# Optimization experiments

Measured on AMD Instinct MI355X. Metric: run time of the kernel, lower is better.

## Reference

```python
import jax, jax.numpy as jnp
import numpy as np

BATCH, LEN, N_STATE, D_MODEL = 16, 512, 64, 256
DT_MIN, DT_MAX = 1e-3, 1e-1


def setup_inputs() -> dict:
    key = jax.random.key(0)
    ks = jax.random.split(key, 8)
    log_dt = jax.random.uniform(ks[7], (1,), jnp.float32) * (np.log(DT_MAX) - np.log(DT_MIN)) + np.log(DT_MIN)
    return {
        "u": jax.random.normal(ks[0], (BATCH, LEN, D_MODEL), jnp.float32),
        "Lambda_re": jax.random.normal(ks[1], (N_STATE,), jnp.float32),
        "Lambda_im": jax.random.normal(ks[2], (N_STATE,), jnp.float32),
        "B_re": jax.random.normal(ks[3], (N_STATE,), jnp.float32),
        "B_im": jax.random.normal(ks[4], (N_STATE,), jnp.float32),
        "P_re": jax.random.normal(ks[5], (N_STATE, D_MODEL), jnp.float32),
        "P_im": jax.random.normal(ks[6], (N_STATE, D_MODEL), jnp.float32),
        "log_dt": log_dt,
    }


def reference(u, Lambda_re, Lambda_im, B_re, B_im, P_re, P_im, log_dt):
    # Diagonal (S4D-style) SSM recurrence, per-channel independent states.
    dt = jnp.exp(log_dt[0])
    Lam = Lambda_re + 1j * Lambda_im                      # (N,)
    a = jnp.exp(dt * (-jnp.exp(Lam)))                     # (N,) discrete diagonal transition
    Bd = (dt * (B_re + 1j * B_im)).astype(jnp.complex64)  # (N,)
    C = (P_re + 1j * P_im).astype(jnp.complex64)          # (N, D)
    a = a.astype(jnp.complex64)

    def step(x, u_t):
        # x: (B, N, D) complex state, u_t: (B, D) real input at this timestep
        x = a[None, :, None] * x + Bd[None, :, None] * u_t[:, None, :].astype(jnp.complex64)
        y = jnp.einsum('nd,bnd->bd', C, x)                # contract state dim
        return x, y

    x0 = jnp.zeros((u.shape[0], a.shape[0], u.shape[2]), dtype=jnp.complex64)
    _, ys = jax.lax.scan(step, x0, jnp.swapaxes(u, 0, 1))  # ys: (L, B, D)
    return jnp.swapaxes(ys, 0, 1).real                     # (B, L, D) float32
```

## Files before the change

### kernel.cpp

```cpp
#include <hip/hip_runtime.h>

#define BATCH  16
#define LEN    512
#define NSTATE 64
#define DMODEL 256
#define TB     32
#define WAVES  4

__global__ __launch_bounds__(WAVES * 64, 4)
void s4d_scan_kernel(const float* __restrict__ u,
                     const float* __restrict__ Lre_p, const float* __restrict__ Lim_p,
                     const float* __restrict__ Bre_p, const float* __restrict__ Bim_p,
                     const float* __restrict__ Pre_p, const float* __restrict__ Pim_p,
                     const float* __restrict__ logdt_p,
                     float* __restrict__ y)
{
    __shared__ float cb[WAVES][NSTATE][TB + 1];

    const int tid  = threadIdx.x;
    const int lane = tid & 63;
    const int widx = tid >> 6;
    const int wid  = blockIdx.x * WAVES + widx;
    const int b    = wid >> 8;
    const int d    = wid & 255;

    const float dt  = expf(logdt_p[0]);
    const float Lre = Lre_p[lane];
    const float Lim = Lim_p[lane];
    const float eL  = expf(Lre);
    const float wre = -eL * cosf(Lim);
    const float wim = -eL * sinf(Lim);
    const float mag = expf(dt * wre);
    const float are = mag * cosf(dt * wim);
    const float aim = mag * sinf(dt * wim);
    const float Bdre = dt * Bre_p[lane];
    const float Bdim = dt * Bim_p[lane];
    const float Pre  = Pre_p[lane * DMODEL + d];
    const float Pim  = Pim_p[lane * DMODEL + d];
    const float Gre = Pre * Bdre - Pim * Bdim;
    const float Gim = Pre * Bdim + Pim * Bdre;

    float zre = 0.f, zim = 0.f;

    const float* up = u + (size_t)b * LEN * DMODEL + d;
    float*       yp = y + (size_t)b * LEN * DMODEL + d;

    const int tl = lane & 31;
    const int h  = lane >> 5;

    for (int t0 = 0; t0 < LEN; t0 += TB) {
        const float ureg = up[(t0 + tl) * DMODEL];

        #pragma unroll
        for (int tau = 0; tau < TB; ++tau) {
            const float us = __uint_as_float(
                __builtin_amdgcn_readlane(__float_as_uint(ureg), tau));
            const float nzre = fmaf(are, zre, fmaf(-aim, zim, Gre * us));
            const float nzim = fmaf(are, zim, fmaf( aim, zre, Gim * us));
            zre = nzre;
            zim = nzim;
            cb[widx][lane][tau] = zre;
        }
        __syncthreads();

        float s = 0.f;
        #pragma unroll
        for (int j = 0; j < 32; ++j)
            s += cb[widx][32 * h + j][tl];
        s += __shfl_xor(s, 32, 64);
        if (lane < 32)
            yp[(t0 + tl) * DMODEL] = s;
        __syncthreads();
    }
}

extern "C" void kernel_launch(void* const* d_in, const int* in_sizes, int n_in,
                              void* d_out, int out_size, void* d_ws, size_t ws_size,
                              hipStream_t stream) {
    const float* u      = (const float*)d_in[0];
    const float* Lre    = (const float*)d_in[1];
    const float* Lim    = (const float*)d_in[2];
    const float* Bre    = (const float*)d_in[3];
    const float* Bim    = (const float*)d_in[4];
    const float* Pre    = (const float*)d_in[5];
    const float* Pim    = (const float*)d_in[6];
    const float* logdt  = (const float*)d_in[7];
    float* y = (float*)d_out;

    const int nblocks = (BATCH * DMODEL) / WAVES;
    s4d_scan_kernel<<<nblocks, WAVES * 64, 0, stream>>>(
        u, Lre, Lim, Bre, Bim, Pre, Pim, logdt, y);
}
```

Baseline: 38.14 us.

## Prefetch next 64-step input chunk, halve waves per block, pad LDS rows by two

Each lane now loads a 64-timestep input chunk and prefetches the next chunk into a register while the current one is scanned, so global load latency overlaps the recurrence. WAVES drops from 4 to 2, which doubles the block count and narrows each __syncthreads barrier. LDS row padding changes from 1 to 2 so pairs of adjacent stores can be merged. The risks are a stride-34 layout that may add bank conflicts on the column reads, and higher register pressure.

Measured after the change: 43.25 us. +13.4%, slower.

```diff
diff --git a/kernel.cpp b/kernel.cpp
--- a/kernel.cpp
+++ b/kernel.cpp
@@ -5,7 +5,8 @@
 #define NSTATE 64
 #define DMODEL 256
 #define TB     32
-#define WAVES  4
+#define WAVES  2
+#define PAD    2
 
 __global__ __launch_bounds__(WAVES * 64, 4)
 void s4d_scan_kernel(const float* __restrict__ u,
@@ -15,7 +16,7 @@
                      const float* __restrict__ logdt_p,
                      float* __restrict__ y)
 {
-    __shared__ float cb[WAVES][NSTATE][TB + 1];
+    __shared__ float cb[WAVES][NSTATE][TB + PAD];
 
     const int tid  = threadIdx.x;
     const int lane = tid & 63;
@@ -48,29 +49,41 @@
     const int tl = lane & 31;
     const int h  = lane >> 5;
 
-    for (int t0 = 0; t0 < LEN; t0 += TB) {
-        const float ureg = up[(t0 + tl) * DMODEL];
+    float ucur = up[lane * DMODEL];
+
+    for (int m = 0; m < LEN / 64; ++m) {
+        float unext = 0.f;
+        if (m + 1 < LEN / 64)
+            unext = up[((m + 1) * 64 + lane) * DMODEL];
 
         #pragma unroll
-        for (int tau = 0; tau < TB; ++tau) {
-            const float us = __uint_as_float(
-                __builtin_amdgcn_readlane(__float_as_uint(ureg), tau));
-            const float nzre = fmaf(are, zre, fmaf(-aim, zim, Gre * us));
-            const float nzim = fmaf(are, zim, fmaf( aim, zre, Gim * us));
-            zre = nzre;
-            zim = nzim;
-            cb[widx][lane][tau] = zre;
+        for (int half = 0; half < 2; ++half) {
+            #pragma unroll
+            for (int tau = 0; tau < TB; tau += 2) {
+                const float us0 = __uint_as_float(
+                    __builtin_amdgcn_readlane(__float_as_uint(ucur), half * 32 + tau));
+                const float r0 = fmaf(are, zre, fmaf(-aim, zim, Gre * us0));
+                const float i0 = fmaf(are, zim, fmaf( aim, zre, Gim * us0));
+                const float us1 = __uint_as_float(
+                    __builtin_amdgcn_readlane(__float_as_uint(ucur), half * 32 + tau + 1));
+                const float r1 = fmaf(are, r0, fmaf(-aim, i0, Gre * us1));
+                const float i1 = fmaf(are, i0, fmaf( aim, r0, Gim * us1));
+                zre = r1; zim = i1;
+                cb[widx][lane][tau]     = r0;
+                cb[widx][lane][tau + 1] = r1;
+            }
+            __syncthreads();
+
+            float s = 0.f;
+            #pragma unroll
+            for (int j = 0; j < 32; ++j)
+                s += cb[widx][32 * h + j][tl];
+            s += __shfl_xor(s, 32, 64);
+            if (lane < 32)
+                yp[(m * 64 + half * 32 + tl) * DMODEL] = s;
+            __syncthreads();
         }
-        __syncthreads();
-
-        float s = 0.f;
-        #pragma unroll
-        for (int j = 0; j < 32; ++j)
-            s += cb[widx][32 * h + j][tl];
-        s += __shfl_xor(s, 32, 64);
-        if (lane < 32)
-            yp[(t0 + tl) * DMODEL] = s;
-        __syncthreads();
+        ucur = unext;
     }
 }
 
```

## Replace sequential SSM scan with precomputed convolution kernel and direct FIR

Applied to the files above, without the earlier changes.

The diagonal SSM recurrence becomes an explicit causal convolution. A first kernel builds K[tau,d] = Re(sum_n C[n,d] * Bd[n] * a[n]^tau) into workspace, and a second kernel computes each output tile of 16 timesteps as a register-blocked FIR over all past inputs. This removes the serial dependency chain along the sequence and the LDS reduction over states. In exchange the FIR does O(L^2) work per channel and load is uneven across tiles, since late tiles loop far longer than early ones. Computing a^tau through exp and sincos rather than repeated multiplication may also shift numerics slightly.

New measurement: 51.26 us. 34.4% more time.

```diff
diff --git a/kernel.cpp b/kernel.cpp
--- a/kernel.cpp
+++ b/kernel.cpp
@@ -1,93 +1,123 @@
 #include <hip/hip_runtime.h>
 
-#define BATCH  16
-#define LEN    512
-#define NSTATE 64
-#define DMODEL 256
-#define TB     32
-#define WAVES  4
+#define B_    16
+#define L_    512
+#define N_    64
+#define D_    256
+#define T_    16
+#define NT    (L_ / T_)
+#define KROWS (L_ + T_)
+#define GUARD 4
 
-__global__ __launch_bounds__(WAVES * 64, 4)
-void s4d_scan_kernel(const float* __restrict__ u,
-                     const float* __restrict__ Lre_p, const float* __restrict__ Lim_p,
-                     const float* __restrict__ Bre_p, const float* __restrict__ Bim_p,
-                     const float* __restrict__ Pre_p, const float* __restrict__ Pim_p,
-                     const float* __restrict__ logdt_p,
-                     float* __restrict__ y)
+__global__ __launch_bounds__(256)
+void build_K(const float* __restrict__ Lre_p, const float* __restrict__ Lim_p,
+             const float* __restrict__ Bre_p, const float* __restrict__ Bim_p,
+             const float* __restrict__ Pre_p, const float* __restrict__ Pim_p,
+             const float* __restrict__ logdt_p,
+             float* __restrict__ Kpad)
 {
-    __shared__ float cb[WAVES][NSTATE][TB + 1];
+    __shared__ float U[N_], V[N_];
+    const int row = blockIdx.x;
+    const int tau = row - T_;
+    const int d   = threadIdx.x;
 
-    const int tid  = threadIdx.x;
-    const int lane = tid & 63;
-    const int widx = tid >> 6;
-    const int wid  = blockIdx.x * WAVES + widx;
-    const int b    = wid >> 8;
-    const int d    = wid & 255;
+    if (tau < 0) {
+        Kpad[row * D_ + d] = 0.f;
+        return;
+    }
 
-    const float dt  = expf(logdt_p[0]);
-    const float Lre = Lre_p[lane];
-    const float Lim = Lim_p[lane];
-    const float eL  = expf(Lre);
-    const float wre = -eL * cosf(Lim);
-    const float wim = -eL * sinf(Lim);
-    const float mag = expf(dt * wre);
-    const float are = mag * cosf(dt * wim);
-    const float aim = mag * sinf(dt * wim);
-    const float Bdre = dt * Bre_p[lane];
-    const float Bdim = dt * Bim_p[lane];
-    const float Pre  = Pre_p[lane * DMODEL + d];
-    const float Pim  = Pim_p[lane * DMODEL + d];
-    const float Gre = Pre * Bdre - Pim * Bdim;
-    const float Gim = Pre * Bdim + Pim * Bdre;
+    const float dt = expf(logdt_p[0]);
+    if (d < N_) {
+        const float Lre = Lre_p[d], Lim = Lim_p[d];
+        const float eL  = expf(Lre);
+        const float wre = -eL * cosf(Lim);
+        const float wim = -eL * sinf(Lim);
+        const float ft  = (float)tau;
+        const float er  = expf(ft * dt * wre);
+        float sn, cs;
+        sincosf(ft * dt * wim, &sn, &cs);
+        const float Ar = er * cs, Ai = er * sn;
+        const float Bdre = dt * Bre_p[d], Bdim = dt * Bim_p[d];
+        U[d] = Bdre * Ar - Bdim * Ai;
+        V[d] = Bdim * Ar + Bdre * Ai;
+    }
+    __syncthreads();
 
-    float zre = 0.f, zim = 0.f;
+    float acc = 0.f;
+    #pragma unroll 8
+    for (int n = 0; n < N_; ++n)
+        acc = fmaf(Pre_p[n * D_ + d], U[n],
+              fmaf(-Pim_p[n * D_ + d], V[n], acc));
+    Kpad[row * D_ + d] = acc;
+}
 
-    const float* up = u + (size_t)b * LEN * DMODEL + d;
-    float*       yp = y + (size_t)b * LEN * DMODEL + d;
+__global__ __launch_bounds__(256)
+void conv_fir(const float* __restrict__ u, const float* __restrict__ Kpad,
+              float* __restrict__ y)
+{
+    const int bid = blockIdx.x;
+    const int k   = (NT - 1) - (bid >> 4);
+    const int b   = bid & (B_ - 1);
+    const int d   = threadIdx.x;
 
-    const int tl = lane & 31;
-    const int h  = lane >> 5;
+    const float* ub = u + ((size_t)b * L_) * D_ + d;
+    const float* Kb = Kpad + d;
+    float*       yb = y + ((size_t)b * L_ + k * T_) * D_ + d;
 
-    for (int t0 = 0; t0 < LEN; t0 += TB) {
-        const float ureg = up[(t0 + tl) * DMODEL];
+    const int send = T_ * (k + 1);
+    const int r0   = T_ * k + T_;
 
+    float W[16];
+    #pragma unroll
+    for (int j = 1; j < 16; ++j) W[j] = Kb[(r0 + j) * D_];
+    float kr[4], ur[4];
+    #pragma unroll
+    for (int p = 0; p < 4; ++p) {
+        kr[p] = Kb[(r0 - p) * D_];
+        ur[p] = ub[p * D_];
+    }
+    float acc[16];
+    #pragma unroll
+    for (int j = 0; j < 16; ++j) acc[j] = 0.f;
+
+    for (int s0 = 0; s0 < send; s0 += 16) {
         #pragma unroll
-        for (int tau = 0; tau < TB; ++tau) {
-            const float us = __uint_as_float(
-                __builtin_amdgcn_readlane(__float_as_uint(ureg), tau));
-            const float nzre = fmaf(are, zre, fmaf(-aim, zim, Gre * us));
-            const float nzim = fmaf(are, zim, fmaf( aim, zre, Gim * us));
-            zre = nzre;
-            zim = nzim;
-            cb[widx][lane][tau] = zre;
+        for (int m = 0; m < 16; ++m) {
+            const float uv = ur[m & 3];
+            const float kv = kr[m & 3];
+            acc[0] = fmaf(kv, uv, acc[0]);
+            #pragma unroll
+            for (int j = 1; j < 16; ++j)
+                acc[j] = fmaf(W[(j - m) & 15], uv, acc[j]);
+            W[(16 - m) & 15] = kv;
+            const int s = s0 + m;
+            kr[m & 3] = Kb[(r0 - s - 4) * D_];
+            const int spf = (s + 4 < L_) ? (s + 4) : (L_ - 1);
+            ur[m & 3] = ub[spf * D_];
         }
-        __syncthreads();
+    }
 
-        float s = 0.f;
-        #pragma unroll
-        for (int j = 0; j < 32; ++j)
-            s += cb[widx][32 * h + j][tl];
-        s += __shfl_xor(s, 32, 64);
-        if (lane < 32)
-            yp[(t0 + tl) * DMODEL] = s;
-        __syncthreads();
-    }
+    #pragma unroll
+    for (int j = 0; j < 16; ++j)
+        yb[j * D_] = acc[j];
 }
 
 extern "C" void kernel_launch(void* const* d_in, const int* in_sizes, int n_in,
                               void* d_out, int out_size, void* d_ws, size_t ws_size,
                               hipStream_t stream) {
-    const float* u      = (const float*)d_in[0];
-    const float* Lre    = (const float*)d_in[1];
-    const float* Lim    = (const float*)d_in[2];
-    const float* Bre    = (const float*)d_in[3];
-    const float* Bim    = (const float*)d_in[4];
-    const float* Pre    = (const float*)d_in[5];
-    const float* Pim    = (const float*)d_in[6];
-    const float* logdt  = (const float*)d_in[7];
+    const float* u     = (const float*)d_in[0];
+    const float* Lre   = (const float*)d_in[1];
+    const float* Lim   = (const float*)d_in[2];
+    const float* Bre   = (const float*)d_in[3];
+    const float* Bim   = (const float*)d_in[4];
+    const float* Pre   = (const float*)d_in[5];
+    const float* Pim   = (const float*)d_in[6];
+    const float* logdt = (const float*)d_in[7];
     float* y = (float*)d_out;
 
-    const int nblocks = (BATCH * DMODEL) / WAVES;
-    s4d_scan_kernel<<<nblocks, WAVES * 64, 0, stream>>>(
-        u, Lre, Lim, Bre, Bim, Pre, Pim, logdt, y);
+    float* Kpad0 = (float*)d_ws;
+    float* Kpad  = Kpad0 + GUARD * D_;
+
+    build_K<<<KROWS, 256, 0, stream>>>(Lre, Lim, Bre, Bim, Pre, Pim, logdt, Kpad);
+    conv_fir<<<B_ * NT, 256, 0, stream>>>(u, Kpad, y);
 }
```

## Replace LDS transpose reduction with per-step DPP wave reduction and writelane packing

Applied to the files above, without the earlier changes.

Drops the shared-memory buffer and both block-wide barriers. Each timestep's state sum is now reduced across the 64 lanes with a DPP butterfly/row-broadcast chain, read out via readlane, and 32 results are packed into one vector register with v_writelane for a coalesced store. Input loads are also double-buffered by prefetching the next 64-timestep chunk. The cost is about six DPP adds plus a readlane on the serial recurrence path for every step, in place of the LDS writes and the batched reduction.

Result: slower. 73.24 us (+92.0%).

```diff
diff --git a/kernel.cpp b/kernel.cpp
--- a/kernel.cpp
+++ b/kernel.cpp
@@ -4,8 +4,14 @@
 #define LEN    512
 #define NSTATE 64
 #define DMODEL 256
-#define TB     32
 #define WAVES  4
+
+template<int CTRL, int RMASK>
+__device__ __forceinline__ float dpp_add(float x) {
+    int t = __builtin_amdgcn_update_dpp(0, __float_as_int(x), CTRL,
+                                        RMASK, 0xf, true);
+    return x + __int_as_float(t);
+}
 
 __global__ __launch_bounds__(WAVES * 64, 4)
 void s4d_scan_kernel(const float* __restrict__ u,
@@ -15,8 +21,6 @@
                      const float* __restrict__ logdt_p,
                      float* __restrict__ y)
 {
-    __shared__ float cb[WAVES][NSTATE][TB + 1];
-
     const int tid  = threadIdx.x;
     const int lane = tid & 63;
     const int widx = tid >> 6;
@@ -46,31 +50,51 @@
     float*       yp = y + (size_t)b * LEN * DMODEL + d;
 
     const int tl = lane & 31;
-    const int h  = lane >> 5;
 
-    for (int t0 = 0; t0 < LEN; t0 += TB) {
-        const float ureg = up[(t0 + tl) * DMODEL];
+    float ucur = up[lane * DMODEL];
+
+    for (int m = 0; m < LEN / 64; ++m) {
+        const int mn = (m + 1) & (LEN / 64 - 1);
+        float unext = up[(mn * 64 + lane) * DMODEL];
 
         #pragma unroll
-        for (int tau = 0; tau < TB; ++tau) {
-            const float us = __uint_as_float(
-                __builtin_amdgcn_readlane(__float_as_uint(ureg), tau));
-            const float nzre = fmaf(are, zre, fmaf(-aim, zim, Gre * us));
-            const float nzim = fmaf(are, zim, fmaf( aim, zre, Gim * us));
-            zre = nzre;
-            zim = nzim;
-            cb[widx][lane][tau] = zre;
+        for (int half = 0; half < 2; ++half) {
+            unsigned sy[32];
+            #pragma unroll
+            for (int tau = 0; tau < 32; ++tau) {
+                const float us = __uint_as_float(
+                    __builtin_amdgcn_readlane(__float_as_uint(ucur),
+                                              half * 32 + tau));
+                const float nzre = fmaf(are, zre, fmaf(-aim, zim, Gre * us));
+                const float nzim = fmaf(are, zim, fmaf( aim, zre, Gim * us));
+                zre = nzre;
+                zim = nzim;
+
+                float s = zre;
+                s = dpp_add<0x0B1, 0xf>(s);
+                s = dpp_add<0x04E, 0xf>(s);
+                s = dpp_add<0x141, 0xf>(s);
+                s = dpp_add<0x140, 0xf>(s);
+                s = dpp_add<0x142, 0xa>(s);
+                s = dpp_add<0x143, 0xc>(s);
+                sy[tau] = __builtin_amdgcn_readlane(__float_as_uint(s), 63);
+            }
+
+            unsigned vy = 0u;
+#define WLANE(J) asm("v_writelane_b32 %0, %1, " #J : "+v"(vy) : "s"(sy[J]));
+            WLANE(0)  WLANE(1)  WLANE(2)  WLANE(3)
+            WLANE(4)  WLANE(5)  WLANE(6)  WLANE(7)
+            WLANE(8)  WLANE(9)  WLANE(10) WLANE(11)
+            WLANE(12) WLANE(13) WLANE(14) WLANE(15)
+            WLANE(16) WLANE(17) WLANE(18) WLANE(19)
+            WLANE(20) WLANE(21) WLANE(22) WLANE(23)
+            WLANE(24) WLANE(25) WLANE(26) WLANE(27)
+            WLANE(28) WLANE(29) WLANE(30) WLANE(31)
+#undef WLANE
+            if (lane < 32)
+                yp[(m * 64 + half * 32 + tl) * DMODEL] = __uint_as_float(vy);
         }
-        __syncthreads();
-
-        float s = 0.f;
-        #pragma unroll
-        for (int j = 0; j < 32; ++j)
-            s += cb[widx][32 * h + j][tl];
-        s += __shfl_xor(s, 32, 64);
-        if (lane < 32)
-            yp[(t0 + tl) * DMODEL] = s;
-        __syncthreads();
+        ucur = unext;
     }
 }
 
```
